# Kernel optimization log

Measured on AMD Instinct MI355X. Metric: run time of the kernel, lower is better.

Reference implementation:

```python
import jax, jax.numpy as jnp
import numpy as np

H, N, OUT = 1024, 64, 512  # channels, SSM state size, output feats


def posenc3d(f, h, w, channels):
    # standard positional_encodings.PositionalEncoding3D
    ch = int(np.ceil(channels / 6) * 2)  # per-axis channels (342 for 1024)
    inv_freq = jnp.asarray(1.0 / (10000.0 ** (np.arange(0, ch, 2, dtype=np.float32) / ch)))

    def emb(n):
        s = jnp.arange(n, dtype=jnp.float32)[:, None] * inv_freq[None, :]  # (n, ch/2)
        return jnp.stack([jnp.sin(s), jnp.cos(s)], axis=-1).reshape(n, -1)  # interleaved (n, ch)

    ex, ey, ez = emb(f), emb(h), emb(w)
    pe = jnp.zeros((f, h, w, ch * 3), dtype=jnp.float32)
    pe = pe.at[..., :ch].set(ex[:, None, None, :])
    pe = pe.at[..., ch:2 * ch].set(ey[None, :, None, :])
    pe = pe.at[..., 2 * ch:].set(ez[None, None, :, :])
    return pe[..., :channels]  # truncate 3*342=1026 -> 1024


def s4_kernel(log_dt, A_re, A_im, C_re, C_im, L):
    # S4D ZOH kernel: K[h,l] = 2*Re( sum_n C'[h,n] * exp(dt_h*A[h,n]*l) )
    dt = jnp.exp(log_dt)                      # (H,)
    A = A_re + 1j * A_im                      # (H,N)
    C = C_re + 1j * C_im                      # (H,N)
    dtA = dt[:, None] * A                     # (H,N)
    Ct = C * (jnp.exp(dtA) - 1.0) / A         # discretized C' (H,N)
    l = jnp.arange(L, dtype=jnp.float32)

    def body(acc, xs):  # scan over state dim to avoid (H,N,L) materialization
        ct, da = xs  # (H,), (H,)
        return acc + ct[:, None] * jnp.exp(da[:, None] * l), None

    acc0 = jnp.zeros((log_dt.shape[0], L), dtype=jnp.complex64)
    K, _ = jax.lax.scan(body, acc0, (Ct.T, dtA.T))
    return 2.0 * K.real  # (H, L)


def reference(x, log_dt, A_re, A_im, C_re, C_im, D, W_out, b_out):
    bs, ch, f, h, w = x.shape
    L = f * h * w
    u = jnp.transpose(x, (0, 2, 3, 4, 1))                 # bs f h w ch
    u = u + posenc3d(f, h, w, ch)[None]
    u = u.reshape(bs, L, ch)
    v = jnp.transpose(u, (0, 2, 1))                       # (bs, ch, L)
    K = s4_kernel(log_dt, A_re, A_im, C_re, C_im, L)      # (ch, L)
    # causal FFT convolution (pad to 2L)
    Uf = jnp.fft.rfft(v, 2 * L)
    Kf = jnp.fft.rfft(K, 2 * L)
    y = jnp.fft.irfft(Uf * Kf[None], 2 * L)[..., :L]
    y = y + D[None, :, None] * v                          # skip connection
    y = jax.nn.gelu(jnp.transpose(y, (0, 2, 1)))          # (bs, L, ch)
    out = y @ W_out + b_out                               # (bs, L, OUT)
    return jnp.transpose(out, (0, 2, 1)).reshape(bs, W_out.shape[1], f, h, w)


def setup_inputs() -> dict:
    key = jax.random.key(0)
    ks = jax.random.split(key, 6)
    bs, f, h, w = 2, 16, 16, 16
    x = jax.random.normal(ks[0], (bs, H, f, h, w), dtype=jnp.float32)
    # S4D-Lin init
    log_dt = jax.random.uniform(ks[1], (H,), dtype=jnp.float32) * (np.log(0.1) - np.log(0.001)) + np.log(0.001)
    A_re = -0.5 * jnp.ones((H, N), dtype=jnp.float32)
    A_im = jnp.broadcast_to(np.pi * jnp.arange(N, dtype=jnp.float32)[None, :], (H, N)).copy()
    C_re = jax.random.normal(ks[2], (H, N), dtype=jnp.float32) * (0.5 ** 0.5)
    C_im = jax.random.normal(ks[3], (H, N), dtype=jnp.float32) * (0.5 ** 0.5)
    D = jax.random.normal(ks[4], (H,), dtype=jnp.float32)
    W_out = jax.random.normal(ks[5], (H, OUT), dtype=jnp.float32) / np.float32(np.sqrt(H))
    b_out = jnp.zeros((OUT,), dtype=jnp.float32)
    return {"x": x, "log_dt": log_dt, "A_re": A_re, "A_im": A_im, "C_re": C_re,
            "C_im": C_im, "D": D, "W_out": W_out, "b_out": b_out}
```

## Files before the change

kernel.cpp:

```cpp
#include <hip/hip_runtime.h>
#include <cstdint>
#include <cstddef>

#define H_CH 1024
#define OUTF 512
#define LSEQ 4096

typedef __bf16 bf16x8 __attribute__((ext_vector_type(8)));
typedef float floatx4 __attribute__((ext_vector_type(4)));

__device__ __forceinline__ unsigned short f2bf(float f) {
    __bf16 b = (__bf16)f;
    return __builtin_bit_cast(unsigned short, b);
}
__device__ __forceinline__ unsigned int pack2(float a, float b) {
    return (unsigned int)f2bf(a) | ((unsigned int)f2bf(b) << 16);
}
__device__ __forceinline__ float bf2f(unsigned short u) {
    unsigned int x = ((unsigned int)u) << 16;
    return __builtin_bit_cast(float, x);
}
struct c32 { float x, y; };
__device__ __forceinline__ c32 cmul(c32 a, c32 b) {
    return { fmaf(a.x, b.x, -a.y * b.y), fmaf(a.x, b.y, a.y * b.x) };
}
__device__ __forceinline__ c32 cpow16(c32 a, int w) {
    c32 p = {1.f, 0.f};
    if (w) {
        c32 a2 = cmul(a, a), a4 = cmul(a2, a2), a8 = cmul(a4, a4), a16 = cmul(a8, a8);
        p = a16;
        for (int k = 1; k < w; ++k) p = cmul(p, a16);
    }
    return p;
}
__device__ __forceinline__ float gelu_fast(float y) {
    float u = y + 0.044715f * y * y * y;
    float e = __expf(-1.5957691216057308f * u);
    return y * __builtin_amdgcn_rcpf(1.f + e);
}

__global__ __launch_bounds__(256) void coef_kernel(
    const float* __restrict__ log_dt, const float* __restrict__ A_re,
    const float* __restrict__ A_im, const float* __restrict__ C_re,
    const float* __restrict__ C_im, float* __restrict__ coef)
{
    const int i = blockIdx.x * 256 + threadIdx.x;
    const int c = i >> 6;
    double are = A_re[i], aim = A_im[i], cre = C_re[i], cim = C_im[i];
    double dt  = exp((double)log_dt[c]);
    double dar = dt * are, dai = dt * aim;
    double er = exp(dar), cd = cos(dai), sd = sin(dai);
    double lre = er * cd, limm = er * sd;
    double ei = exp(-dar);
    double eQ = exp(64.0 * dar), cQ = cos(64.0 * dai), sQ = sin(64.0 * dai);
    double nre = lre - 1.0, nim = limm;
    double d2  = are * are + aim * aim;
    double qre = (nre * are + nim * aim) / d2;
    double qim = (nim * are - nre * aim) / d2;
    double ctre = cre * qre - cim * qim, ctim = cre * qim + cim * qre;
    float4 w0 = make_float4((float)lre, (float)limm, (float)(ei * cd), (float)(-ei * sd));
    float4 w1 = make_float4((float)(eQ * cQ), (float)(eQ * sQ),
                            (float)(2.0 * ctre), (float)(-2.0 * ctim));
    *(float4*)&coef[(size_t)i * 8]     = w0;
    *(float4*)&coef[(size_t)i * 8 + 4] = w1;
}

__global__ __launch_bounds__(256) void s4_fused_kernel(
    const float* __restrict__ x, const float* __restrict__ coef,
    const float* __restrict__ Dp, unsigned short* __restrict__ gprime)
{
    __shared__ __align__(16) unsigned short Vs[64 * 72];
    __shared__ __align__(16) unsigned short Ps[65 * 136];
    __shared__ __align__(16) unsigned char  RY[128 * 72 * 2];
    __shared__ __align__(16) unsigned short Ss[64 * 136];
    __shared__ __align__(16) unsigned short Ts[64 * 72];
    __shared__ float2 Es[4][64];
    __shared__ float  pe16[16];
    unsigned short* Fs   = (unsigned short*)RY;
    unsigned short* Rs   = (unsigned short*)RY;
    unsigned int*   ybuf = (unsigned int*)RY;

    const int c = blockIdx.x;
    const int t = threadIdx.x, lane = t & 63, w = t >> 6, n = lane;
    const int lm = lane & 15, lq = lane >> 4;

    const int axis = (c >= 684) ? 2 : ((c >= 342) ? 1 : 0);
    const int j = c - 342 * axis;
    const int is_cos = j & 1;
    if (t < 16) {
        const float freq = (float)exp(-log(10000.0) * (double)(2 * (j >> 1)) / 342.0);
        float a = (float)t * freq;
        pe16[t] = is_cos ? cosf(a) : sinf(a);
    }
    const float* cf = coef + ((size_t)c * 64 + n) * 8;
    c32 lam = {cf[0], cf[1]}, inv = {cf[2], cf[3]}, lamQ = {cf[4], cf[5]};
    const float c2r = cf[6], c2mi = cf[7];
    const float Dc = Dp[c];
    __syncthreads();

    auto deltascan = [&](int bb) {
        const float* xp = x + ((size_t)bb * H_CH + c) * (size_t)LSEQ;
        #pragma unroll
        for (int r = 0; r < 2; ++r) {
            const int i = r * 256 + t, l0 = i * 8;
            float4 f0 = *(const float4*)(xp + l0);
            float4 f1 = *(const float4*)(xp + l0 + 4);
            float e[8] = {f0.x, f0.y, f0.z, f0.w, f1.x, f1.y, f1.z, f1.w};
            unsigned int o[4];
            #pragma unroll
            for (int k = 0; k < 4; ++k) {
                const int la = l0 + 2 * k, lb = la + 1;
                const int pa = axis == 0 ? (la >> 8) : axis == 1 ? ((la >> 4) & 15) : (la & 15);
                const int pb = axis == 0 ? (lb >> 8) : axis == 1 ? ((lb >> 4) & 15) : (lb & 15);
                o[k] = pack2(e[2 * k] + pe16[pa], e[2 * k + 1] + pe16[pb]);
            }
            *(uint4*)&Vs[(i >> 3) * 72 + (i & 7) * 8] = make_uint4(o[0], o[1], o[2], o[3]);
        }
        {
            c32 l2 = cmul(lam, lam), l4 = cmul(l2, l2), l8 = cmul(l4, l4);
            c32 l16 = cmul(l8, l8), l32 = cmul(l16, l16);
            c32 z = cmul(cmul(cmul(cmul(cmul(l32, l16), l8), l4), l2), lam);
            z = cmul(z, cpow16(inv, w));
            #pragma unroll
            for (int s = 0; s < 16; ++s) {
                const int u = 16 * w + s;
                Fs[(2 * n) * 72 + u]     = f2bf(z.x);
                Fs[(2 * n + 1) * 72 + u] = f2bf(z.y);
                z = cmul(z, inv);
            }
        }
        __syncthreads();
        {
            floatx4 acc[2][4];
            #pragma unroll
            for (int a = 0; a < 2; ++a)
                #pragma unroll
                for (int b = 0; b < 4; ++b) acc[a][b] = (floatx4){0.f, 0.f, 0.f, 0.f};
            #pragma unroll
            for (int kt = 0; kt < 2; ++kt) {
                bf16x8 a0 = *(const bf16x8*)&Fs[(32 * w + lm) * 72 + kt * 32 + lq * 8];
                bf16x8 a1 = *(const bf16x8*)&Fs[(32 * w + 16 + lm) * 72 + kt * 32 + lq * 8];
                #pragma unroll
                for (int nt = 0; nt < 4; ++nt) {
                    bf16x8 b = *(const bf16x8*)&Vs[(nt * 16 + lm) * 72 + kt * 32 + lq * 8];
                    acc[0][nt] = __builtin_amdgcn_mfma_f32_16x16x32_bf16(a0, b, acc[0][nt], 0, 0, 0);
                    acc[1][nt] = __builtin_amdgcn_mfma_f32_16x16x32_bf16(a1, b, acc[1][nt], 0, 0, 0);
                }
            }
            #pragma unroll
            for (int sm = 0; sm < 2; ++sm)
                #pragma unroll
                for (int nt = 0; nt < 4; ++nt) {
                    const int row = 32 * w + sm * 16 + lq * 4, col = nt * 16 + lm;
                    *(uint2*)&Ss[col * 136 + row] =
                        make_uint2(pack2(acc[sm][nt][0], acc[sm][nt][1]),
                                   pack2(acc[sm][nt][2], acc[sm][nt][3]));
                }
        }
        __syncthreads();
        {
            float sr = 0.f, si = 0.f;
            #pragma unroll
            for (int jc = 0; jc < 16; ++jc) {
                unsigned int d = *(unsigned int*)&Ss[(16 * w + jc) * 136 + 2 * n];
                float dr = bf2f((unsigned short)(d & 0xffff));
                float di = bf2f((unsigned short)(d >> 16));
                float nr = fmaf(lamQ.x, sr, fmaf(-lamQ.y, si, dr));
                float ni = fmaf(lamQ.x, si, fmaf(lamQ.y, sr, di));
                sr = nr; si = ni;
            }
            Es[w][n] = make_float2(sr, si);
        }
        __syncthreads();
        {
            c32 Q2 = cmul(lamQ, lamQ), Q4 = cmul(Q2, Q2), Q8 = cmul(Q4, Q4);
            c32 Q16 = cmul(Q8, Q8);
            float cr = 0.f, ci = 0.f;
            for (int w2 = 0; w2 < w; ++w2) {
                float2 e = Es[w2][n];
                float nr = fmaf(Q16.x, cr, fmaf(-Q16.y, ci, e.x));
                float ni = fmaf(Q16.x, ci, fmaf(Q16.y, cr, e.y));
                cr = nr; ci = ni;
            }
            float sr = cr, si = ci;
            #pragma unroll
            for (int jc = 0; jc < 16; ++jc) {
                unsigned int* p = (unsigned int*)&Ss[(16 * w + jc) * 136 + 2 * n];
                unsigned int d = *p;
                *p = pack2(sr, si);
                float dr = bf2f((unsigned short)(d & 0xffff));
                float di = bf2f((unsigned short)(d >> 16));
                float nr = fmaf(lamQ.x, sr, fmaf(-lamQ.y, si, dr));
                float ni = fmaf(lamQ.x, si, fmaf(lamQ.y, sr, di));
                sr = nr; si = ni;
            }
        }
        __syncthreads();
    };

    auto gemm2_epi = [&](int bb) {
        floatx4 a2[4];
        #pragma unroll
        for (int nt = 0; nt < 4; ++nt) a2[nt] = (floatx4){0.f, 0.f, 0.f, 0.f};
        #pragma unroll
        for (int kt = 0; kt < 2; ++kt) {
            bf16x8 a = *(const bf16x8*)&Ts[(16 * w + lm) * 72 + kt * 32 + lq * 8];
            #pragma unroll
            for (int nt = 0; nt < 4; ++nt) {
                bf16x8 b = *(const bf16x8*)&Vs[(nt * 16 + lm) * 72 + kt * 32 + lq * 8];
                a2[nt] = __builtin_amdgcn_mfma_f32_16x16x32_bf16(a, b, a2[nt], 0, 0, 0);
            }
        }
        #pragma unroll
        for (int kt = 0; kt < 4; ++kt) {
            bf16x8 a = *(const bf16x8*)&Ps[(16 * w + lm + 1) * 136 + kt * 32 + lq * 8];
            #pragma unroll
            for (int nt = 0; nt < 4; ++nt) {
                bf16x8 b = *(const bf16x8*)&Ss[(nt * 16 + lm) * 136 + kt * 32 + lq * 8];
                a2[nt] = __builtin_amdgcn_mfma_f32_16x16x32_bf16(a, b, a2[nt], 0, 0, 0);
            }
        }
        __syncthreads();
        #pragma unroll
        for (int nt = 0; nt < 4; ++nt) {
            const int chunk = nt * 16 + lm;
            float gg[4];
            #pragma unroll
            for (int r = 0; r < 4; ++r) {
                const int tt = 16 * w + lq * 4 + r;
                const float vv = bf2f(Vs[chunk * 72 + tt]);
                gg[r] = gelu_fast(fmaf(Dc, vv, a2[nt][r]));
            }
            const int p0 = 8 * w + 2 * lq;
            ybuf[chunk * 34 + p0]     = pack2(gg[0], gg[1]);
            ybuf[chunk * 34 + p0 + 1] = pack2(gg[2], gg[3]);
        }
        __syncthreads();
        unsigned int* gp = (unsigned int*)gprime
                         + (size_t)bb * 32 * 1024 * 64 + (size_t)c * 64;
        #pragma unroll
        for (int q = 0; q < 8; ++q) {
            const int idx = q * 256 + t;
            const int lt = idx >> 6, w32 = idx & 63;
            gp[(size_t)lt * (1024 * 64) + w32] = ybuf[(idx >> 5) * 34 + (idx & 31)];
        }
        __syncthreads();
    };

    deltascan(0);

    {
        c32 z = cmul((c32){c2r, -c2mi}, cpow16(lam, w));
        const int steps = (w == 3) ? 17 : 16;
        for (int s = 0; s < steps; ++s) {
            const int tt = 16 * w + s;
            *(unsigned int*)&Ps[tt * 136 + 2 * n] = pack2(z.x, -z.y);
            z = cmul(z, lam);
        }
    }
    {
        c32 z = cpow16(inv, w);
        #pragma unroll
        for (int s = 0; s < 16; ++s) {
            const int u = 16 * w + s;
            *(unsigned int*)&Rs[u * 136 + 2 * n] = pack2(z.x, z.y);
            z = cmul(z, inv);
        }
    }
    __syncthreads();
    {
        floatx4 a1[4];
        #pragma unroll
        for (int nt = 0; nt < 4; ++nt) a1[nt] = (floatx4){0.f, 0.f, 0.f, 0.f};
        #pragma unroll
        for (int kt = 0; kt < 4; ++kt) {
            bf16x8 a = *(const bf16x8*)&Ps[(16 * w + lm) * 136 + kt * 32 + lq * 8];
            #pragma unroll
            for (int nt = 0; nt < 4; ++nt) {
                bf16x8 b = *(const bf16x8*)&Rs[(nt * 16 + lm) * 136 + kt * 32 + lq * 8];
                a1[nt] = __builtin_amdgcn_mfma_f32_16x16x32_bf16(a, b, a1[nt], 0, 0, 0);
            }
        }
        #pragma unroll
        for (int nt = 0; nt < 4; ++nt)
            #pragma unroll
            for (int r = 0; r < 4; ++r) {
                const int row = 16 * w + lq * 4 + r, col = nt * 16 + lm;
                Ts[row * 72 + col] = f2bf(row >= col ? a1[nt][r] : 0.f);
            }
    }
    __syncthreads();

    gemm2_epi(0);
    deltascan(1);
    gemm2_epi(1);
}

__global__ __launch_bounds__(256) void transpose_w_kernel(
    const float* __restrict__ W, unsigned short* __restrict__ Wt)
{
    __shared__ float tileF[64 * 65];
    const int t = threadIdx.x;
    const int o0 = blockIdx.x * 64, k0 = blockIdx.y * 64;
    {
        const int ty = t >> 6, tx = t & 63;
        #pragma unroll
        for (int r = 0; r < 16; ++r) {
            const int ki = r * 4 + ty;
            tileF[ki * 65 + tx] = W[(size_t)(k0 + ki) * OUTF + o0 + tx];
        }
    }
    __syncthreads();
    {
        const int ty = t >> 5, tx = t & 31;
        #pragma unroll
        for (int r = 0; r < 8; ++r) {
            const int oi = r * 8 + ty;
            unsigned int u0 = f2bf(tileF[(2 * tx) * 65 + oi]);
            unsigned int u1 = f2bf(tileF[(2 * tx + 1) * 65 + oi]);
            *(unsigned int*)&Wt[(size_t)(o0 + oi) * H_CH + k0 + 2 * tx] = u0 | (u1 << 16);
        }
    }
}

__global__ __launch_bounds__(256) void gemm_kernel(
    const unsigned short* __restrict__ gp, const unsigned short* __restrict__ Wt,
    const float* __restrict__ b_out, float* __restrict__ out)
{
    __shared__ unsigned short As[64 * 40];
    __shared__ unsigned short Bs[128 * 40];
    const int t = threadIdx.x, lane = t & 63, w = t >> 6;
    const int lm = lane & 15, lq = lane >> 4;
    const int bx = blockIdx.x;
    const int o0 = blockIdx.y * 64;
    const int bb = blockIdx.z;
    const int l0 = bx * 128;
    const unsigned short* bsrc = gp + (size_t)(bb * 32 + bx) * (1024 * 128);

    const int arow = t >> 2, aq = t & 3;
    const int bp = t & 15, bgq = t >> 4;

    uint4 areg, breg0, breg1;
    {
        areg  = *(const uint4*)(Wt + (size_t)(o0 + arow) * H_CH + aq * 8);
        const unsigned short* b0 = bsrc + (size_t)(2 * bp) * 128 + bgq * 8;
        breg0 = *(const uint4*)(b0);
        breg1 = *(const uint4*)(b0 + 128);
    }

    floatx4 acc[4][2];
    #pragma unroll
    for (int i = 0; i < 4; ++i)
        #pragma unroll
        for (int jj = 0; jj < 2; ++jj) acc[i][jj] = (floatx4){0.f, 0.f, 0.f, 0.f};

    for (int kt = 0; kt < 32; ++kt) {
        if (kt) __syncthreads();
        *(uint4*)&As[arow * 40 + aq * 8] = areg;
        {
            unsigned int* bu = (unsigned int*)Bs;
            const unsigned int* a = (const unsigned int*)&breg0;
            const unsigned int* b = (const unsigned int*)&breg1;
            #pragma unroll
            for (int i = 0; i < 4; ++i) {
                unsigned int lo = (a[i] & 0xffffu) | (b[i] << 16);
                unsigned int hi = (a[i] >> 16) | (b[i] & 0xffff0000u);
                bu[(bgq * 8 + 2 * i) * 20 + bp]     = lo;
                bu[(bgq * 8 + 2 * i + 1) * 20 + bp] = hi;
            }
        }
        __syncthreads();
        if (kt < 31) {
            const int k0 = (kt + 1) * 32;
            areg  = *(const uint4*)(Wt + (size_t)(o0 + arow) * H_CH + k0 + aq * 8);
            const unsigned short* b0 = bsrc + (size_t)(k0 + 2 * bp) * 128 + bgq * 8;
            breg0 = *(const uint4*)(b0);
            breg1 = *(const uint4*)(b0 + 128);
        }

        bf16x8 af[4], bfr[2];
        #pragma unroll
        for (int sm = 0; sm < 4; ++sm)
            af[sm] = *(const bf16x8*)&As[(sm * 16 + lm) * 40 + lq * 8];
        #pragma unroll
        for (int sn = 0; sn < 2; ++sn)
            bfr[sn] = *(const bf16x8*)&Bs[(w * 32 + sn * 16 + lm) * 40 + lq * 8];
        #pragma unroll
        for (int sm = 0; sm < 4; ++sm)
            #pragma unroll
            for (int sn = 0; sn < 2; ++sn)
                acc[sm][sn] = __builtin_amdgcn_mfma_f32_16x16x32_bf16(
                    af[sm], bfr[sn], acc[sm][sn], 0, 0, 0);
    }

    #pragma unroll
    for (int sm = 0; sm < 4; ++sm)
        #pragma unroll
        for (int sn = 0; sn < 2; ++sn)
            #pragma unroll
            for (int r = 0; r < 4; ++r) {
                const int o = o0 + sm * 16 + lq * 4 + r;
                const int l = l0 + w * 32 + sn * 16 + lm;
                out[((size_t)bb * OUTF + o) * LSEQ + l] = acc[sm][sn][r] + b_out[o];
            }
}

extern "C" void kernel_launch(void* const* d_in, const int* in_sizes, int n_in,
                              void* d_out, int out_size, void* d_ws, size_t ws_size,
                              hipStream_t stream) {
    const float* x      = (const float*)d_in[0];
    const float* log_dt = (const float*)d_in[1];
    const float* A_re   = (const float*)d_in[2];
    const float* A_im   = (const float*)d_in[3];
    const float* C_re   = (const float*)d_in[4];
    const float* C_im   = (const float*)d_in[5];
    const float* Dp     = (const float*)d_in[6];
    const float* W_out  = (const float*)d_in[7];
    const float* b_out  = (const float*)d_in[8];
    float* out = (float*)d_out;

    char* ws = (char*)d_ws;
    unsigned short* gprime = (unsigned short*)ws;
    unsigned short* Wt     = (unsigned short*)(ws + (size_t)17 * 1024 * 1024);
    float*          coef   = (float*)(ws + (size_t)19 * 1024 * 1024);

    coef_kernel<<<256, 256, 0, stream>>>(log_dt, A_re, A_im, C_re, C_im, coef);
    s4_fused_kernel<<<1024, 256, 0, stream>>>(x, coef, Dp, gprime);
    transpose_w_kernel<<<dim3(8, 16), 256, 0, stream>>>(W_out, Wt);
    gemm_kernel<<<dim3(32, 8, 2), 256, 0, stream>>>(gprime, Wt, b_out, out);
}
```

Before: 146.4 us.

## Merge coef and W transpose into one prep kernel, deepen GEMM K-tile

```diff
diff --git a/kernel.cpp b/kernel.cpp
--- a/kernel.cpp
+++ b/kernel.cpp
@@ -39,30 +39,57 @@
     return y * __builtin_amdgcn_rcpf(1.f + e);
 }
 
-__global__ __launch_bounds__(256) void coef_kernel(
+__global__ __launch_bounds__(256) void prep_kernel(
     const float* __restrict__ log_dt, const float* __restrict__ A_re,
     const float* __restrict__ A_im, const float* __restrict__ C_re,
-    const float* __restrict__ C_im, float* __restrict__ coef)
+    const float* __restrict__ C_im, const float* __restrict__ W,
+    float* __restrict__ coef, unsigned short* __restrict__ Wt)
 {
-    const int i = blockIdx.x * 256 + threadIdx.x;
-    const int c = i >> 6;
-    double are = A_re[i], aim = A_im[i], cre = C_re[i], cim = C_im[i];
-    double dt  = exp((double)log_dt[c]);
-    double dar = dt * are, dai = dt * aim;
-    double er = exp(dar), cd = cos(dai), sd = sin(dai);
-    double lre = er * cd, limm = er * sd;
-    double ei = exp(-dar);
-    double eQ = exp(64.0 * dar), cQ = cos(64.0 * dai), sQ = sin(64.0 * dai);
-    double nre = lre - 1.0, nim = limm;
-    double d2  = are * are + aim * aim;
-    double qre = (nre * are + nim * aim) / d2;
-    double qim = (nim * are - nre * aim) / d2;
-    double ctre = cre * qre - cim * qim, ctim = cre * qim + cim * qre;
-    float4 w0 = make_float4((float)lre, (float)limm, (float)(ei * cd), (float)(-ei * sd));
-    float4 w1 = make_float4((float)(eQ * cQ), (float)(eQ * sQ),
-                            (float)(2.0 * ctre), (float)(-2.0 * ctim));
-    *(float4*)&coef[(size_t)i * 8]     = w0;
-    *(float4*)&coef[(size_t)i * 8 + 4] = w1;
+    __shared__ float tileF[64 * 65];
+    const int t = threadIdx.x;
+    if (blockIdx.x < 256) {
+        const int i = blockIdx.x * 256 + t;
+        const int c = i >> 6;
+        double are = A_re[i], aim = A_im[i], cre = C_re[i], cim = C_im[i];
+        double dt  = exp((double)log_dt[c]);
+        double dar = dt * are, dai = dt * aim;
+        double er = exp(dar), cd = cos(dai), sd = sin(dai);
+        double lre = er * cd, limm = er * sd;
+        double ei = exp(-dar);
+        double eQ = exp(64.0 * dar), cQ = cos(64.0 * dai), sQ = sin(64.0 * dai);
+        double nre = lre - 1.0, nim = limm;
+        double d2  = are * are + aim * aim;
+        double qre = (nre * are + nim * aim) / d2;
+        double qim = (nim * are - nre * aim) / d2;
+        double ctre = cre * qre - cim * qim, ctim = cre * qim + cim * qre;
+        float4 w0 = make_float4((float)lre, (float)limm, (float)(ei * cd), (float)(-ei * sd));
+        float4 w1 = make_float4((float)(eQ * cQ), (float)(eQ * sQ),
+                                (float)(2.0 * ctre), (float)(-2.0 * ctim));
+        *(float4*)&coef[(size_t)i * 8]     = w0;
+        *(float4*)&coef[(size_t)i * 8 + 4] = w1;
+    } else {
+        const int bid = blockIdx.x - 256;
+        const int o0 = (bid & 7) * 64, k0 = (bid >> 3) * 64;
+        {
+            const int ty = t >> 6, tx = t & 63;
+            #pragma unroll
+            for (int r = 0; r < 16; ++r) {
+                const int ki = r * 4 + ty;
+                tileF[ki * 65 + tx] = W[(size_t)(k0 + ki) * OUTF + o0 + tx];
+            }
+        }
+        __syncthreads();
+        {
+            const int ty = t >> 5, tx = t & 31;
+            #pragma unroll
+            for (int r = 0; r < 8; ++r) {
+                const int oi = r * 8 + ty;
+                unsigned int u0 = f2bf(tileF[(2 * tx) * 65 + oi]);
+                unsigned int u1 = f2bf(tileF[(2 * tx + 1) * 65 + oi]);
+                *(unsigned int*)&Wt[(size_t)(o0 + oi) * H_CH + k0 + 2 * tx] = u0 | (u1 << 16);
+            }
+        }
+    }
 }
 
 __global__ __launch_bounds__(256) void s4_fused_kernel(
@@ -96,6 +123,16 @@
     c32 lam = {cf[0], cf[1]}, inv = {cf[2], cf[3]}, lamQ = {cf[4], cf[5]};
     const float c2r = cf[6], c2mi = cf[7];
     const float Dc = Dp[c];
+
+    unsigned int fz[16];
+    {
+        c32 l2 = cmul(lam, lam), l4 = cmul(l2, l2), l8 = cmul(l4, l4);
+        c32 l16 = cmul(l8, l8), l32 = cmul(l16, l16);
+        c32 z = cmul(cmul(cmul(cmul(cmul(l32, l16), l8), l4), l2), lam);
+        z = cmul(z, cpow16(inv, w));
+        #pragma unroll
+        for (int s = 0; s < 16; ++s) { fz[s] = pack2(z.x, z.y); z = cmul(z, inv); }
+    }
     __syncthreads();
 
     auto deltascan = [&](int bb) {
@@ -116,18 +153,11 @@
             }
             *(uint4*)&Vs[(i >> 3) * 72 + (i & 7) * 8] = make_uint4(o[0], o[1], o[2], o[3]);
         }
-        {
-            c32 l2 = cmul(lam, lam), l4 = cmul(l2, l2), l8 = cmul(l4, l4);
-            c32 l16 = cmul(l8, l8), l32 = cmul(l16, l16);
-            c32 z = cmul(cmul(cmul(cmul(cmul(l32, l16), l8), l4), l2), lam);
-            z = cmul(z, cpow16(inv, w));
-            #pragma unroll
-            for (int s = 0; s < 16; ++s) {
-                const int u = 16 * w + s;
-                Fs[(2 * n) * 72 + u]     = f2bf(z.x);
-                Fs[(2 * n + 1) * 72 + u] = f2bf(z.y);
-                z = cmul(z, inv);
-            }
+        #pragma unroll
+        for (int s = 0; s < 16; ++s) {
+            const int u = 16 * w + s;
+            Fs[(2 * n) * 72 + u]     = (unsigned short)(fz[s] & 0xffffu);
+            Fs[(2 * n + 1) * 72 + u] = (unsigned short)(fz[s] >> 16);
         }
         __syncthreads();
         {
@@ -296,57 +326,37 @@
     gemm2_epi(1);
 }
 
-__global__ __launch_bounds__(256) void transpose_w_kernel(
-    const float* __restrict__ W, unsigned short* __restrict__ Wt)
-{
-    __shared__ float tileF[64 * 65];
-    const int t = threadIdx.x;
-    const int o0 = blockIdx.x * 64, k0 = blockIdx.y * 64;
-    {
-        const int ty = t >> 6, tx = t & 63;
-        #pragma unroll
-        for (int r = 0; r < 16; ++r) {
-            const int ki = r * 4 + ty;
-            tileF[ki * 65 + tx] = W[(size_t)(k0 + ki) * OUTF + o0 + tx];
-        }
-    }
-    __syncthreads();
-    {
-        const int ty = t >> 5, tx = t & 31;
-        #pragma unroll
-        for (int r = 0; r < 8; ++r) {
-            const int oi = r * 8 + ty;
-            unsigned int u0 = f2bf(tileF[(2 * tx) * 65 + oi]);
-            unsigned int u1 = f2bf(tileF[(2 * tx + 1) * 65 + oi]);
-            *(unsigned int*)&Wt[(size_t)(o0 + oi) * H_CH + k0 + 2 * tx] = u0 | (u1 << 16);
-        }
-    }
-}
-
 __global__ __launch_bounds__(256) void gemm_kernel(
     const unsigned short* __restrict__ gp, const unsigned short* __restrict__ Wt,
     const float* __restrict__ b_out, float* __restrict__ out)
 {
-    __shared__ unsigned short As[64 * 40];
-    __shared__ unsigned short Bs[128 * 40];
+    __shared__ unsigned short As[64 * 72];
+    __shared__ unsigned short Bs[128 * 72];
     const int t = threadIdx.x, lane = t & 63, w = t >> 6;
     const int lm = lane & 15, lq = lane >> 4;
-    const int bx = blockIdx.x;
-    const int o0 = blockIdx.y * 64;
+    const int o0 = blockIdx.x * 64;
+    const int by = blockIdx.y;
     const int bb = blockIdx.z;
-    const int l0 = bx * 128;
-    const unsigned short* bsrc = gp + (size_t)(bb * 32 + bx) * (1024 * 128);
-
-    const int arow = t >> 2, aq = t & 3;
-    const int bp = t & 15, bgq = t >> 4;
-
-    uint4 areg, breg0, breg1;
-    {
-        areg  = *(const uint4*)(Wt + (size_t)(o0 + arow) * H_CH + aq * 8);
-        const unsigned short* b0 = bsrc + (size_t)(2 * bp) * 128 + bgq * 8;
-        breg0 = *(const uint4*)(b0);
-        breg1 = *(const uint4*)(b0 + 128);
-    }
+    const int l0 = by * 128;
+    const unsigned short* bsrc = gp + (size_t)(bb * 32 + by) * (1024 * 128);
+
+    const int kp = t & 31, bg = t >> 5;
+
+    uint4 aR[2], bR[4];
+    auto loadA = [&](int k0) {
+        #pragma unroll
+        for (int h = 0; h < 2; ++h) {
+            const int idx = t + h * 256, row = idx >> 3, q = idx & 7;
+            aR[h] = *(const uint4*)(Wt + (size_t)(o0 + row) * H_CH + k0 + q * 8);
+        }
+    };
+    auto loadB = [&](int k0) {
+        const unsigned short* s0 = bsrc + (size_t)(k0 + 2 * kp) * 128 + bg * 16;
+        bR[0] = *(const uint4*)(s0);
+        bR[1] = *(const uint4*)(s0 + 8);
+        bR[2] = *(const uint4*)(s0 + 128);
+        bR[3] = *(const uint4*)(s0 + 136);
+    };
 
     floatx4 acc[4][2];
     #pragma unroll
@@ -354,43 +364,53 @@
         #pragma unroll
         for (int jj = 0; jj < 2; ++jj) acc[i][jj] = (floatx4){0.f, 0.f, 0.f, 0.f};
 
-    for (int kt = 0; kt < 32; ++kt) {
+    loadA(0); loadB(0);
+    for (int kt = 0; kt < 16; ++kt) {
         if (kt) __syncthreads();
-        *(uint4*)&As[arow * 40 + aq * 8] = areg;
+        {
+            #pragma unroll
+            for (int h = 0; h < 2; ++h) {
+                const int idx = t + h * 256, row = idx >> 3, q = idx & 7;
+                *(uint4*)&As[row * 72 + q * 8] = aR[h];
+            }
+        }
         {
             unsigned int* bu = (unsigned int*)Bs;
-            const unsigned int* a = (const unsigned int*)&breg0;
-            const unsigned int* b = (const unsigned int*)&breg1;
+            const unsigned int* a0 = (const unsigned int*)&bR[0];
+            const unsigned int* a1 = (const unsigned int*)&bR[1];
+            const unsigned int* b0 = (const unsigned int*)&bR[2];
+            const unsigned int* b1 = (const unsigned int*)&bR[3];
             #pragma unroll
             for (int i = 0; i < 4; ++i) {
-                unsigned int lo = (a[i] & 0xffffu) | (b[i] << 16);
-                unsigned int hi = (a[i] >> 16) | (b[i] & 0xffff0000u);
-                bu[(bgq * 8 + 2 * i) * 20 + bp]     = lo;
-                bu[(bgq * 8 + 2 * i + 1) * 20 + bp] = hi;
-            }
-        }
-        __syncthreads();
-        if (kt < 31) {
-            const int k0 = (kt + 1) * 32;
-            areg  = *(const uint4*)(Wt + (size_t)(o0 + arow) * H_CH + k0 + aq * 8);
-            const unsigned short* b0 = bsrc + (size_t)(k0 + 2 * bp) * 128 + bgq * 8;
-            breg0 = *(const uint4*)(b0);
-            breg1 = *(const uint4*)(b0 + 128);
-        }
-
-        bf16x8 af[4], bfr[2];
-        #pragma unroll
-        for (int sm = 0; sm < 4; ++sm)
-            af[sm] = *(const bf16x8*)&As[(sm * 16 + lm) * 40 + lq * 8];
-        #pragma unroll
-        for (int sn = 0; sn < 2; ++sn)
-            bfr[sn] = *(const bf16x8*)&Bs[(w * 32 + sn * 16 + lm) * 40 + lq * 8];
-        #pragma unroll
-        for (int sm = 0; sm < 4; ++sm)
+                unsigned int lo0 = (a0[i] & 0xffffu) | (b0[i] << 16);
+                unsigned int hi0 = (a0[i] >> 16) | (b0[i] & 0xffff0000u);
+                unsigned int lo1 = (a1[i] & 0xffffu) | (b1[i] << 16);
+                unsigned int hi1 = (a1[i] >> 16) | (b1[i] & 0xffff0000u);
+                bu[(bg * 16 + 2 * i) * 36 + kp]     = lo0;
+                bu[(bg * 16 + 2 * i + 1) * 36 + kp] = hi0;
+                bu[(bg * 16 + 8 + 2 * i) * 36 + kp]     = lo1;
+                bu[(bg * 16 + 8 + 2 * i + 1) * 36 + kp] = hi1;
+            }
+        }
+        __syncthreads();
+        if (kt < 15) { loadA((kt + 1) * 64); loadB((kt + 1) * 64); }
+
+        #pragma unroll
+        for (int q2 = 0; q2 < 2; ++q2) {
+            bf16x8 af[4], bfr[2];
+            #pragma unroll
+            for (int sm = 0; sm < 4; ++sm)
+                af[sm] = *(const bf16x8*)&As[(sm * 16 + lm) * 72 + q2 * 32 + lq * 8];
             #pragma unroll
             for (int sn = 0; sn < 2; ++sn)
-                acc[sm][sn] = __builtin_amdgcn_mfma_f32_16x16x32_bf16(
-                    af[sm], bfr[sn], acc[sm][sn], 0, 0, 0);
+                bfr[sn] = *(const bf16x8*)&Bs[(w * 32 + sn * 16 + lm) * 72 + q2 * 32 + lq * 8];
+            #pragma unroll
+            for (int sm = 0; sm < 4; ++sm)
+                #pragma unroll
+                for (int sn = 0; sn < 2; ++sn)
+                    acc[sm][sn] = __builtin_amdgcn_mfma_f32_16x16x32_bf16(
+                        af[sm], bfr[sn], acc[sm][sn], 0, 0, 0);
+        }
     }
 
     #pragma unroll
@@ -424,8 +444,8 @@
     unsigned short* Wt     = (unsigned short*)(ws + (size_t)17 * 1024 * 1024);
     float*          coef   = (float*)(ws + (size_t)19 * 1024 * 1024);
 
-    coef_kernel<<<256, 256, 0, stream>>>(log_dt, A_re, A_im, C_re, C_im, coef);
+    prep_kernel<<<384, 256, 0, stream>>>(log_dt, A_re, A_im, C_re, C_im, W_out,
+                                         coef, Wt);
     s4_fused_kernel<<<1024, 256, 0, stream>>>(x, coef, Dp, gprime);
-    transpose_w_kernel<<<dim3(8, 16), 256, 0, stream>>>(W_out, Wt);
-    gemm_kernel<<<dim3(32, 8, 2), 256, 0, stream>>>(gprime, Wt, b_out, out);
-}
+    gemm_kernel<<<dim3(8, 32, 2), 256, 0, stream>>>(gprime, Wt, b_out, out);
+}
```

Measured after the change: 151.3 us. +3.3%, slower.
